# Optimization experiments

Hardware: AMD Instinct MI355X
Metric: run time of the kernel (lower is better)

## Reference

```python
import jax, jax.numpy as jnp
import numpy as np

N, E, IN_DIM, HID, OUT = 50000, 600000, 128, 256, 128

def setup_inputs() -> dict:
    key = jax.random.key(0)
    k1, k2, k3, k4, k5, k6, k7 = jax.random.split(key, 7)
    h = jax.random.normal(k1, (N, IN_DIM), dtype=jnp.float32)
    src = jax.random.randint(k2, (E,), 0, N)
    dst = jax.random.randint(k3, (E,), 0, N)
    s1 = 1.0 / np.sqrt(2 * IN_DIM)
    s2 = 1.0 / np.sqrt(HID)
    W1 = jax.random.uniform(k4, (2 * IN_DIM, HID), minval=-s1, maxval=s1, dtype=jnp.float32)
    b1 = jax.random.uniform(k5, (HID,), minval=-s1, maxval=s1, dtype=jnp.float32)
    W2 = jax.random.uniform(k6, (HID, OUT), minval=-s2, maxval=s2, dtype=jnp.float32)
    b2 = jax.random.uniform(k7, (OUT,), minval=-s2, maxval=s2, dtype=jnp.float32)
    return {"h": h, "src": src, "dst": dst, "W1": W1, "b1": b1, "W2": W2, "b2": b2}

def reference(h, src, dst, W1, b1, W2, b2):
    n = h.shape[0]
    # copy_u + mean: gather src features, segment-sum at dst, divide by in-degree
    msg_sum = jax.ops.segment_sum(h[src], dst, num_segments=n)          # [N, D]
    deg = jax.ops.segment_sum(jnp.ones((src.shape[0],), h.dtype), dst, num_segments=n)
    h_neigh = msg_sum / jnp.maximum(deg, 1.0)[:, None]                  # zero-deg nodes -> 0
    h_total = jnp.concatenate([h, h_neigh], axis=1)                     # [N, 2D]
    out = (h_total @ W1 + b1) @ W2 + b2                                 # 2-layer MLP (no inner activation)
    return jax.nn.relu(out)
```

## Files before the change

### kernel.cpp

```cpp
#include <hip/hip_runtime.h>

#define N_NODES 50000
#define E_EDGES 600000
#define IN_DIM  128
#define HID     256
#define OUT_DIM 128
#define CAP     64

typedef __bf16 bf16x8 __attribute__((ext_vector_type(8)));
typedef float  f32x16 __attribute__((ext_vector_type(16)));

__device__ __forceinline__ unsigned short f2bf(float f) {
    union { float f; unsigned int i; } v; v.f = f;
    unsigned int b = v.i;
    b += 0x7fffu + ((b >> 16) & 1u);
    return (unsigned short)(b >> 16);
}
__device__ __forceinline__ float bf2f(unsigned short u) {
    union { unsigned int i; float f; } v; v.i = ((unsigned int)u) << 16; return v.f;
}

__global__ void sage_fill(const int* __restrict__ src,
                          const int* __restrict__ dst,
                          int* __restrict__ counts,
                          int* __restrict__ bucket) {
    int e = blockIdx.x * blockDim.x + threadIdx.x;
    if (e >= E_EDGES) return;
    int d = dst[e];
    int slot = atomicAdd(counts + d, 1);
    if (slot < CAP) bucket[(size_t)d * CAP + slot] = src[e];
}

__global__ void sage_hcvt(const float* __restrict__ h, unsigned short* __restrict__ ht) {
    int idx = blockIdx.x * 256 + threadIdx.x;
    if (idx >= N_NODES * 32) return;
    int n = idx >> 5, g = idx & 31;
    const float4 v = *(const float4*)(h + (size_t)n * IN_DIM + g * 4);
    ushort4 o;
    o.x = f2bf(v.x); o.y = f2bf(v.y); o.z = f2bf(v.z); o.w = f2bf(v.w);
    *(ushort4*)(ht + (size_t)n * 256 + g * 4) = o;
}

__global__ void sage_wcvt(const float* __restrict__ W1, const float* __restrict__ W2,
                          unsigned short* __restrict__ w1sw, unsigned short* __restrict__ w2sw) {
    int i = blockIdx.x * 256 + threadIdx.x;
    if (i < 65536) {
        int j = i & 7, n = (i >> 3) & 255, g = (i >> 11) & 1, ks = (i >> 12) & 3, c = i >> 14;
        int k = c * 64 + ks * 16 + g * 8 + j;
        w1sw[i] = f2bf(W1[(size_t)k * HID + n]);
    } else {
        int i2 = i - 65536;
        if (i2 < 32768) {
            int j = i2 & 7, n = (i2 >> 3) & 127, g = (i2 >> 10) & 1, ks = (i2 >> 11) & 7, c = (i2 >> 14) & 1;
            int k = c * 128 + ks * 16 + g * 8 + j;
            w2sw[i2] = f2bf(W2[(size_t)k * OUT_DIM + n]);
        }
    }
}

__global__ void __launch_bounds__(256)
sage_gather(const int* __restrict__ counts,
            const int* __restrict__ bucket,
            unsigned short* ht) {
    int node = blockIdx.x * 8 + (threadIdx.x >> 5);
    int l = threadIdx.x & 31;
    if (node >= N_NODES) return;

    int dg = counts[node];
    int entries = min(dg, CAP);
    const int* bk = bucket + (size_t)node * CAP;

    float a0 = 0.f, a1 = 0.f, a2 = 0.f, a3 = 0.f;
    int e = 0;
    for (; e + 4 <= entries; e += 4) {
        const int4 s = *(const int4*)(bk + e);
        const ushort4 v0 = *(const ushort4*)(ht + (size_t)s.x * 256 + l * 4);
        const ushort4 v1 = *(const ushort4*)(ht + (size_t)s.y * 256 + l * 4);
        const ushort4 v2 = *(const ushort4*)(ht + (size_t)s.z * 256 + l * 4);
        const ushort4 v3 = *(const ushort4*)(ht + (size_t)s.w * 256 + l * 4);
        a0 += bf2f(v0.x) + bf2f(v1.x) + bf2f(v2.x) + bf2f(v3.x);
        a1 += bf2f(v0.y) + bf2f(v1.y) + bf2f(v2.y) + bf2f(v3.y);
        a2 += bf2f(v0.z) + bf2f(v1.z) + bf2f(v2.z) + bf2f(v3.z);
        a3 += bf2f(v0.w) + bf2f(v1.w) + bf2f(v2.w) + bf2f(v3.w);
    }
    for (; e < entries; ++e) {
        const ushort4 v = *(const ushort4*)(ht + (size_t)bk[e] * 256 + l * 4);
        a0 += bf2f(v.x); a1 += bf2f(v.y); a2 += bf2f(v.z); a3 += bf2f(v.w);
    }
    float inv = 1.0f / (float)max(dg, 1);
    ushort4 o;
    o.x = f2bf(a0 * inv); o.y = f2bf(a1 * inv);
    o.z = f2bf(a2 * inv); o.w = f2bf(a3 * inv);
    *(ushort4*)(ht + (size_t)node * 256 + 128 + l * 4) = o;
}

__global__ void __launch_bounds__(256)
sage_mlp(const unsigned short* ht,
         const unsigned short* __restrict__ w1sw,
         const unsigned short* __restrict__ w2sw,
         const float* __restrict__ b1,
         const float* __restrict__ b2,
         float* out) {
    __shared__ unsigned short wbuf[16384];
    __shared__ unsigned short hid_s[32][264];

    const int t = threadIdx.x;
    const int nw = t >> 6;
    const int lane = t & 63;
    const int lr = lane & 31;
    const int lg = lane >> 5;
    const int base = blockIdx.x * 32;
    const int row_c = min(base + lr, N_NODES - 1);

    bf16x8 a[16];
    {
        const unsigned short* ap = ht + (size_t)row_c * 256 + lg * 8;
        #pragma unroll
        for (int ks = 0; ks < 16; ++ks)
            a[ks] = *(const bf16x8*)(ap + ks * 16);
    }

    f32x16 c1[2];
    #pragma unroll
    for (int e = 0; e < 16; ++e) { c1[0][e] = 0.f; c1[1][e] = 0.f; }

    #pragma unroll
    for (int c = 0; c < 4; ++c) {
        if (c) __syncthreads();
        {
            const bf16x8* gsrc = (const bf16x8*)(w1sw + c * 16384);
            #pragma unroll
            for (int i = 0; i < 8; ++i) {
                int off16 = i * 256 + t;
                *(bf16x8*)(wbuf + off16 * 8) = gsrc[off16];
            }
        }
        __syncthreads();
        #pragma unroll
        for (int ks = 0; ks < 4; ++ks) {
            #pragma unroll
            for (int nt = 0; nt < 2; ++nt) {
                int n = nw * 64 + nt * 32 + lr;
                bf16x8 b = *(const bf16x8*)(wbuf + (((ks * 2 + lg) * 256) + n) * 8);
                c1[nt] = __builtin_amdgcn_mfma_f32_32x32x16_bf16(a[c * 4 + ks], b, c1[nt], 0, 0, 0);
            }
        }
    }

    #pragma unroll
    for (int nt = 0; nt < 2; ++nt) {
        int col = nw * 64 + nt * 32 + lr;
        float bias = b1[col];
        #pragma unroll
        for (int reg = 0; reg < 16; ++reg) {
            int m = (reg & 3) + 8 * (reg >> 2) + 4 * lg;
            hid_s[m][col] = f2bf(c1[nt][reg] + bias);
        }
    }
    __syncthreads();

    f32x16 c2;
    #pragma unroll
    for (int e = 0; e < 16; ++e) c2[e] = 0.f;

    #pragma unroll
    for (int c = 0; c < 2; ++c) {
        if (c) __syncthreads();
        {
            const bf16x8* gsrc = (const bf16x8*)(w2sw + c * 16384);
            #pragma unroll
            for (int i = 0; i < 8; ++i) {
                int off16 = i * 256 + t;
                *(bf16x8*)(wbuf + off16 * 8) = gsrc[off16];
            }
        }
        __syncthreads();
        #pragma unroll
        for (int ks = 0; ks < 8; ++ks) {
            bf16x8 ah = *(const bf16x8*)(&hid_s[lr][c * 128 + ks * 16 + lg * 8]);
            bf16x8 b  = *(const bf16x8*)(wbuf + ((ks * 2 + lg) * 128 + nw * 32 + lr) * 8);
            c2 = __builtin_amdgcn_mfma_f32_32x32x16_bf16(ah, b, c2, 0, 0, 0);
        }
    }

    {
        int col = nw * 32 + lr;
        float bias = b2[col];
        #pragma unroll
        for (int reg = 0; reg < 16; ++reg) {
            int m = (reg & 3) + 8 * (reg >> 2) + 4 * lg;
            int n = base + m;
            if (n < N_NODES)
                out[(size_t)n * OUT_DIM + col] = fmaxf(c2[reg] + bias, 0.0f);
        }
    }
}

extern "C" void kernel_launch(void* const* d_in, const int* in_sizes, int n_in,
                              void* d_out, int out_size, void* d_ws, size_t ws_size,
                              hipStream_t stream) {
    const float* h   = (const float*)d_in[0];
    const int*   src = (const int*)d_in[1];
    const int*   dst = (const int*)d_in[2];
    const float* W1  = (const float*)d_in[3];
    const float* b1  = (const float*)d_in[4];
    const float* W2  = (const float*)d_in[5];
    const float* b2  = (const float*)d_in[6];
    float* out = (float*)d_out;

    unsigned short* ht = (unsigned short*)d_out;

    int* counts = (int*)d_ws;
    int* bucket = counts + N_NODES;
    unsigned short* w1sw = (unsigned short*)(bucket + (size_t)N_NODES * CAP);
    unsigned short* w2sw = w1sw + 65536;

    hipMemsetAsync(counts, 0, N_NODES * sizeof(int), stream);

    sage_fill<<<(E_EDGES + 255) / 256, 256, 0, stream>>>(src, dst, counts, bucket);

    sage_hcvt<<<(N_NODES * 32 + 255) / 256, 256, 0, stream>>>(h, ht);

    sage_wcvt<<<(65536 + 32768 + 255) / 256, 256, 0, stream>>>(W1, W2, w1sw, w2sw);

    sage_gather<<<(N_NODES + 7) / 8, 256, 0, stream>>>(counts, bucket, ht);

    sage_mlp<<<(N_NODES + 31) / 32, 256, 0, stream>>>(ht, w1sw, w2sw, b1, b2, out);
}
```

Before: 185.1 us.

## Fuse prep kernels into one launch and process 64 rows per MLP block

Merges the edge bucketing, feature conversion and weight conversion kernels into a single launch dispatched by block index, which removes two kernel launches. The MLP kernel now handles 64 rows per block with two row tiles, so each weight chunk staged in shared memory feeds twice as many MFMAs. Per-chunk A loads replace preloading all 16 fragments. The cost is more shared memory and accumulator registers, which may reduce occupancy.

```diff
diff --git a/kernel.cpp b/kernel.cpp
--- a/kernel.cpp
+++ b/kernel.cpp
@@ -7,6 +7,10 @@
 #define OUT_DIM 128
 #define CAP     64
 
+#define NB_FILL 2344
+#define NB_HCVT 6250
+#define NB_WCVT 384
+
 typedef __bf16 bf16x8 __attribute__((ext_vector_type(8)));
 typedef float  f32x16 __attribute__((ext_vector_type(16)));
 
@@ -20,37 +24,37 @@
     union { unsigned int i; float f; } v; v.i = ((unsigned int)u) << 16; return v.f;
 }
 
-__global__ void sage_fill(const int* __restrict__ src,
-                          const int* __restrict__ dst,
-                          int* __restrict__ counts,
-                          int* __restrict__ bucket) {
-    int e = blockIdx.x * blockDim.x + threadIdx.x;
-    if (e >= E_EDGES) return;
-    int d = dst[e];
-    int slot = atomicAdd(counts + d, 1);
-    if (slot < CAP) bucket[(size_t)d * CAP + slot] = src[e];
-}
-
-__global__ void sage_hcvt(const float* __restrict__ h, unsigned short* __restrict__ ht) {
-    int idx = blockIdx.x * 256 + threadIdx.x;
-    if (idx >= N_NODES * 32) return;
-    int n = idx >> 5, g = idx & 31;
-    const float4 v = *(const float4*)(h + (size_t)n * IN_DIM + g * 4);
-    ushort4 o;
-    o.x = f2bf(v.x); o.y = f2bf(v.y); o.z = f2bf(v.z); o.w = f2bf(v.w);
-    *(ushort4*)(ht + (size_t)n * 256 + g * 4) = o;
-}
-
-__global__ void sage_wcvt(const float* __restrict__ W1, const float* __restrict__ W2,
-                          unsigned short* __restrict__ w1sw, unsigned short* __restrict__ w2sw) {
-    int i = blockIdx.x * 256 + threadIdx.x;
-    if (i < 65536) {
-        int j = i & 7, n = (i >> 3) & 255, g = (i >> 11) & 1, ks = (i >> 12) & 3, c = i >> 14;
-        int k = c * 64 + ks * 16 + g * 8 + j;
-        w1sw[i] = f2bf(W1[(size_t)k * HID + n]);
+__global__ void __launch_bounds__(256)
+sage_prep(const int* __restrict__ src, const int* __restrict__ dst,
+          int* __restrict__ counts, int* __restrict__ bucket,
+          const float* __restrict__ h, unsigned short* __restrict__ ht,
+          const float* __restrict__ W1, const float* __restrict__ W2,
+          unsigned short* __restrict__ w1sw, unsigned short* __restrict__ w2sw) {
+    int b = blockIdx.x;
+    if (b < NB_FILL) {
+        int e = b * 256 + threadIdx.x;
+        if (e < E_EDGES) {
+            int d = dst[e];
+            int slot = atomicAdd(counts + d, 1);
+            if (slot < CAP) bucket[(size_t)d * CAP + slot] = src[e];
+        }
+    } else if (b < NB_FILL + NB_HCVT) {
+        int idx = (b - NB_FILL) * 256 + threadIdx.x;
+        if (idx < N_NODES * 32) {
+            int n = idx >> 5, g = idx & 31;
+            const float4 v = *(const float4*)(h + (size_t)n * IN_DIM + g * 4);
+            ushort4 o;
+            o.x = f2bf(v.x); o.y = f2bf(v.y); o.z = f2bf(v.z); o.w = f2bf(v.w);
+            *(ushort4*)(ht + (size_t)n * 256 + g * 4) = o;
+        }
     } else {
-        int i2 = i - 65536;
-        if (i2 < 32768) {
+        int i = (b - NB_FILL - NB_HCVT) * 256 + threadIdx.x;
+        if (i < 65536) {
+            int j = i & 7, n = (i >> 3) & 255, g = (i >> 11) & 1, ks = (i >> 12) & 3, c = i >> 14;
+            int k = c * 64 + ks * 16 + g * 8 + j;
+            w1sw[i] = f2bf(W1[(size_t)k * HID + n]);
+        } else {
+            int i2 = i - 65536;
             int j = i2 & 7, n = (i2 >> 3) & 127, g = (i2 >> 10) & 1, ks = (i2 >> 11) & 7, c = (i2 >> 14) & 1;
             int k = c * 128 + ks * 16 + g * 8 + j;
             w2sw[i2] = f2bf(W2[(size_t)k * OUT_DIM + n]);
@@ -102,27 +106,22 @@
          const float* __restrict__ b2,
          float* out) {
     __shared__ unsigned short wbuf[16384];
-    __shared__ unsigned short hid_s[32][264];
+    __shared__ unsigned short hid_s[64][264];
 
     const int t = threadIdx.x;
     const int nw = t >> 6;
     const int lane = t & 63;
     const int lr = lane & 31;
     const int lg = lane >> 5;
-    const int base = blockIdx.x * 32;
-    const int row_c = min(base + lr, N_NODES - 1);
-
-    bf16x8 a[16];
-    {
-        const unsigned short* ap = ht + (size_t)row_c * 256 + lg * 8;
-        #pragma unroll
-        for (int ks = 0; ks < 16; ++ks)
-            a[ks] = *(const bf16x8*)(ap + ks * 16);
-    }
-
-    f32x16 c1[2];
-    #pragma unroll
-    for (int e = 0; e < 16; ++e) { c1[0][e] = 0.f; c1[1][e] = 0.f; }
+    const int base = blockIdx.x * 64;
+    const int row0 = min(base + lr,      N_NODES - 1);
+    const int row1 = min(base + 32 + lr, N_NODES - 1);
+
+    f32x16 c1[2][2];
+    #pragma unroll
+    for (int e = 0; e < 16; ++e) {
+        c1[0][0][e] = 0.f; c1[0][1][e] = 0.f; c1[1][0][e] = 0.f; c1[1][1][e] = 0.f;
+    }
 
     #pragma unroll
     for (int c = 0; c < 4; ++c) {
@@ -135,6 +134,13 @@
                 *(bf16x8*)(wbuf + off16 * 8) = gsrc[off16];
             }
         }
+        bf16x8 a0[4], a1[4];
+        #pragma unroll
+        for (int ks = 0; ks < 4; ++ks) {
+            int koff = (c * 4 + ks) * 16 + lg * 8;
+            a0[ks] = *(const bf16x8*)(ht + (size_t)row0 * 256 + koff);
+            a1[ks] = *(const bf16x8*)(ht + (size_t)row1 * 256 + koff);
+        }
         __syncthreads();
         #pragma unroll
         for (int ks = 0; ks < 4; ++ks) {
@@ -142,7 +148,8 @@
             for (int nt = 0; nt < 2; ++nt) {
                 int n = nw * 64 + nt * 32 + lr;
                 bf16x8 b = *(const bf16x8*)(wbuf + (((ks * 2 + lg) * 256) + n) * 8);
-                c1[nt] = __builtin_amdgcn_mfma_f32_32x32x16_bf16(a[c * 4 + ks], b, c1[nt], 0, 0, 0);
+                c1[0][nt] = __builtin_amdgcn_mfma_f32_32x32x16_bf16(a0[ks], b, c1[0][nt], 0, 0, 0);
+                c1[1][nt] = __builtin_amdgcn_mfma_f32_32x32x16_bf16(a1[ks], b, c1[1][nt], 0, 0, 0);
             }
         }
     }
@@ -152,16 +159,19 @@
         int col = nw * 64 + nt * 32 + lr;
         float bias = b1[col];
         #pragma unroll
-        for (int reg = 0; reg < 16; ++reg) {
-            int m = (reg & 3) + 8 * (reg >> 2) + 4 * lg;
-            hid_s[m][col] = f2bf(c1[nt][reg] + bias);
+        for (int s = 0; s < 2; ++s) {
+            #pragma unroll
+            for (int reg = 0; reg < 16; ++reg) {
+                int m = s * 32 + (reg & 3) + 8 * (reg >> 2) + 4 * lg;
+                hid_s[m][col] = f2bf(c1[s][nt][reg] + bias);
+            }
         }
     }
     __syncthreads();
 
-    f32x16 c2;
-    #pragma unroll
-    for (int e = 0; e < 16; ++e) c2[e] = 0.f;
+    f32x16 c2[2];
+    #pragma unroll
+    for (int e = 0; e < 16; ++e) { c2[0][e] = 0.f; c2[1][e] = 0.f; }
 
     #pragma unroll
     for (int c = 0; c < 2; ++c) {
@@ -177,9 +187,12 @@
         __syncthreads();
         #pragma unroll
         for (int ks = 0; ks < 8; ++ks) {
-            bf16x8 ah = *(const bf16x8*)(&hid_s[lr][c * 128 + ks * 16 + lg * 8]);
-            bf16x8 b  = *(const bf16x8*)(wbuf + ((ks * 2 + lg) * 128 + nw * 32 + lr) * 8);
-            c2 = __builtin_amdgcn_mfma_f32_32x32x16_bf16(ah, b, c2, 0, 0, 0);
+            bf16x8 b = *(const bf16x8*)(wbuf + ((ks * 2 + lg) * 128 + nw * 32 + lr) * 8);
+            int koff = c * 128 + ks * 16 + lg * 8;
+            bf16x8 ah0 = *(const bf16x8*)(&hid_s[lr][koff]);
+            bf16x8 ah1 = *(const bf16x8*)(&hid_s[32 + lr][koff]);
+            c2[0] = __builtin_amdgcn_mfma_f32_32x32x16_bf16(ah0, b, c2[0], 0, 0, 0);
+            c2[1] = __builtin_amdgcn_mfma_f32_32x32x16_bf16(ah1, b, c2[1], 0, 0, 0);
         }
     }
 
@@ -187,11 +200,14 @@
         int col = nw * 32 + lr;
         float bias = b2[col];
         #pragma unroll
-        for (int reg = 0; reg < 16; ++reg) {
-            int m = (reg & 3) + 8 * (reg >> 2) + 4 * lg;
-            int n = base + m;
-            if (n < N_NODES)
-                out[(size_t)n * OUT_DIM + col] = fmaxf(c2[reg] + bias, 0.0f);
+        for (int s = 0; s < 2; ++s) {
+            #pragma unroll
+            for (int reg = 0; reg < 16; ++reg) {
+                int m = s * 32 + (reg & 3) + 8 * (reg >> 2) + 4 * lg;
+                int n = base + m;
+                if (n < N_NODES)
+                    out[(size_t)n * OUT_DIM + col] = fmaxf(c2[s][reg] + bias, 0.0f);
+            }
         }
     }
 }
@@ -217,13 +233,10 @@
 
     hipMemsetAsync(counts, 0, N_NODES * sizeof(int), stream);
 
-    sage_fill<<<(E_EDGES + 255) / 256, 256, 0, stream>>>(src, dst, counts, bucket);
-
-    sage_hcvt<<<(N_NODES * 32 + 255) / 256, 256, 0, stream>>>(h, ht);
-
-    sage_wcvt<<<(65536 + 32768 + 255) / 256, 256, 0, stream>>>(W1, W2, w1sw, w2sw);
+    sage_prep<<<NB_FILL + NB_HCVT + NB_WCVT, 256, 0, stream>>>(
+        src, dst, counts, bucket, h, ht, W1, W2, w1sw, w2sw);
 
     sage_gather<<<(N_NODES + 7) / 8, 256, 0, stream>>>(counts, bucket, ht);
 
-    sage_mlp<<<(N_NODES + 31) / 32, 256, 0, stream>>>(ht, w1sw, w2sw, b1, b2, out);
-}
+    sage_mlp<<<(N_NODES + 63) / 64, 256, 0, stream>>>(ht, w1sw, w2sw, b1, b2, out);
+}
```

Result: no change. 182.9 us (median of 2 runs) (-1.2%).
